# Kernel optimization log

Hardware: AMD Instinct MI355X
Metric: run time of the kernel (lower is better)

Reference implementation:

```python
import math
import jax, jax.numpy as jnp
import numpy as np

BATCH, SEQ, D_MODEL, NUM_HEADS = 4, 2048, 1024, 16
D_K = D_MODEL // NUM_HEADS


def setup_inputs() -> dict:
    key = jax.random.key(0)
    ks = jax.random.split(key, 11)
    s = 0.02
    inp = {
        'encodings_q': jax.random.normal(ks[0], (BATCH, SEQ, D_MODEL), jnp.float32),
        'encodings_k': jax.random.normal(ks[1], (BATCH, SEQ, D_MODEL), jnp.float32),
        'encodings_v': jax.random.normal(ks[2], (BATCH, SEQ, D_MODEL), jnp.float32),
        # causal mask: True = masked out (matches masked_fill semantics)
        'mask': jnp.broadcast_to(jnp.triu(jnp.ones((SEQ, SEQ), bool), k=1),
                                 (BATCH, SEQ, SEQ)),
        'Wq': jax.random.normal(ks[3], (D_MODEL, D_MODEL), jnp.float32) * s,
        'bq': jnp.zeros((D_MODEL,), jnp.float32),
        'Wk': jax.random.normal(ks[4], (D_MODEL, D_MODEL), jnp.float32) * s,
        'bk': jnp.zeros((D_MODEL,), jnp.float32),
        'Wv': jax.random.normal(ks[5], (D_MODEL, D_MODEL), jnp.float32) * s,
        'bv': jnp.zeros((D_MODEL,), jnp.float32),
        'Wo': jax.random.normal(ks[6], (D_MODEL, D_MODEL), jnp.float32) * s,
        'bo': jnp.zeros((D_MODEL,), jnp.float32),
    }
    return inp


def reference(encodings_q, encodings_k, encodings_v, mask,
              Wq, bq, Wk, bk, Wv, bv, Wo, bo):
    B, S, D = encodings_q.shape
    H, Dk = NUM_HEADS, D_K
    # projections (nn.Linear: x @ W.T + b), split heads -> (B, H, S, Dk)
    q = (encodings_q @ Wq.T + bq).reshape(B, S, H, Dk).transpose(0, 2, 1, 3)
    k = (encodings_k @ Wk.T + bk).reshape(B, S, H, Dk).transpose(0, 2, 1, 3)
    v = (encodings_v @ Wv.T + bv).reshape(B, S, H, Dk).transpose(0, 2, 1, 3)
    scores = jnp.einsum('bhqd,bhkd->bhqk', q, k) / math.sqrt(Dk)
    # mask dim == 3 -> unsqueeze head dim; masked_fill(mask, -1e9)
    scores = jnp.where(mask[:, None, :, :], jnp.float32(-1e9), scores)
    weights = jax.nn.softmax(scores, axis=-1)
    attn = jnp.einsum('bhqk,bhkd->bhqd', weights, v)
    attn = attn.transpose(0, 2, 1, 3).reshape(B, S, D)
    return attn @ Wo.T + bo
```

## Files before the change

### kernel.cpp

```cpp
#include <hip/hip_runtime.h>
#include <hip/hip_bf16.h>
#include <cstdint>

typedef __bf16 bf16;
typedef bf16  bf16x4 __attribute__((ext_vector_type(4)));
typedef bf16  bf16x8 __attribute__((ext_vector_type(8)));
typedef float f32x4  __attribute__((ext_vector_type(4)));

#define MFMA16(a, b, c) __builtin_amdgcn_mfma_f32_16x16x32_bf16((a), (b), (c), 0, 0, 0)

constexpr int BATCH = 4;
constexpr int SEQ   = 2048;
constexpr int DM    = 1024;
constexpr int NH    = 16;
constexpr int DK    = 64;

constexpr float QSCALE = 0.125f * 1.44269504088896340736f;

__device__ __forceinline__ void gld_lds16(const void* g, void* l) {
    __builtin_amdgcn_global_load_lds(
        (const __attribute__((address_space(1))) unsigned int*)(uintptr_t)g,
        (__attribute__((address_space(3))) unsigned int*)(uintptr_t)l,
        16, 0, 0);
}

__device__ __forceinline__ bf16x8 cvt8(const float* __restrict__ p) {
    f32x4 a = *(const f32x4*)p;
    f32x4 b = *(const f32x4*)(p + 4);
    bf16x8 r;
    r[0] = (bf16)a[0]; r[1] = (bf16)a[1]; r[2] = (bf16)a[2]; r[3] = (bf16)a[3];
    r[4] = (bf16)b[0]; r[5] = (bf16)b[1]; r[6] = (bf16)b[2]; r[7] = (bf16)b[3];
    return r;
}

__global__ __launch_bounds__(256)
void cvt_all(const float* __restrict__ xq, const float* __restrict__ xk,
             const float* __restrict__ xv,
             const float* __restrict__ wq, const float* __restrict__ wk,
             const float* __restrict__ wv, const float* __restrict__ wo,
             bf16* __restrict__ X3, bf16* __restrict__ WB)
{
    const int bid = blockIdx.x;
    const float* s;
    bf16* d;
    int local;
    if (bid < 12288) {
        const int which = bid >> 12;
        local = bid & 4095;
        s = (which == 0) ? xq : (which == 1) ? xk : xv;
        d = X3 + (size_t)which * ((size_t)BATCH * SEQ * DM);
    } else {
        const int b2 = bid - 12288;
        const int which = b2 >> 9;
        local = b2 & 511;
        s = (which == 0) ? wq : (which == 1) ? wk : (which == 2) ? wv : wo;
        d = WB + (size_t)which * (size_t)(DM * DM);
    }
    const size_t i = ((size_t)local * 256 + threadIdx.x) * 8;
    *(bf16x8*)(d + i) = cvt8(s + i);
}

__global__ __launch_bounds__(256)
void cvt_x(const float* __restrict__ src, bf16* __restrict__ dst) {
    const size_t i = ((size_t)blockIdx.x * 256 + threadIdx.x) * 8;
    *(bf16x8*)(dst + i) = cvt8(src + i);
}

__global__ __launch_bounds__(256)
void cvt_w4(const float* __restrict__ s0, const float* __restrict__ s1,
            const float* __restrict__ s2, const float* __restrict__ s3,
            bf16* __restrict__ dst) {
    const float* s = (blockIdx.y == 0) ? s0 : (blockIdx.y == 1) ? s1
                   : (blockIdx.y == 2) ? s2 : s3;
    const size_t i = ((size_t)blockIdx.x * 256 + threadIdx.x) * 8;
    *(bf16x8*)(dst + (size_t)blockIdx.y * (1024 * 1024) + i) = cvt8(s + i);
}

template <int MODE>
__device__ __forceinline__
void gemm_core(const bf16* __restrict__ A, const bf16* __restrict__ W,
               const float* __restrict__ bias, void* __restrict__ outp,
               int m0, int n0, bf16* As, bf16* Bs, float oscale)
{
    const int tid  = threadIdx.x;
    const int lane = tid & 63;
    const int wave = tid >> 6;
    const int wm   = (wave >> 1) * 64;
    const int wn   = (wave & 1) * 64;
    const int q4   = lane >> 4;
    const int r    = lane & 15;
    const int srow = lane >> 2;
    const int scol = (((lane & 3) ^ ((lane >> 3) & 3)) << 3);

    f32x4 acc[4][4];
#pragma unroll
    for (int i = 0; i < 4; i++)
#pragma unroll
        for (int j = 0; j < 4; j++) acc[i][j] = (f32x4){0.f, 0.f, 0.f, 0.f};

    const bf16* Ag = A + (size_t)(m0 + wave * 32 + srow) * 1024 + scol;
    const bf16* Wg = W + (size_t)(n0 + wave * 32 + srow) * 1024 + scol;
    const int woff = (wave * 32) * 32;
    constexpr int BUF = 128 * 32;

#define GSTAGE(ks, bsel) do {                                        \
        const int _b = (bsel) * BUF + woff;                          \
        gld_lds16(Ag + (ks) * 32,             As + _b);              \
        gld_lds16(Ag + (ks) * 32 + 16 * 1024, As + _b + 16 * 32);   \
        gld_lds16(Wg + (ks) * 32,             Bs + _b);              \
        gld_lds16(Wg + (ks) * 32 + 16 * 1024, Bs + _b + 16 * 32);   \
    } while (0)

    GSTAGE(0, 0);
    GSTAGE(1, 1);

    const int rsw = (r >> 1) & 3;

    int cur = 0, pre = 2;
    for (int t = 0; t < 32; ++t) {
        if (t < 30) {
            asm volatile("s_waitcnt vmcnt(4) lgkmcnt(0)" ::: "memory");
        } else {
            asm volatile("s_waitcnt vmcnt(0) lgkmcnt(0)" ::: "memory");
        }
        __builtin_amdgcn_s_barrier();

        if (t < 30) GSTAGE(t + 2, pre);

        const bf16* Ar = As + cur * BUF;
        const bf16* Br = Bs + cur * BUF;

        bf16x8 af[4], bfr[4];
#pragma unroll
        for (int i = 0; i < 4; i++)
            af[i] = *(const bf16x8*)&Ar[(wm + i * 16 + r) * 32 + ((q4 ^ rsw) << 3)];
#pragma unroll
        for (int j = 0; j < 4; j++)
            bfr[j] = *(const bf16x8*)&Br[(wn + j * 16 + r) * 32 + ((q4 ^ rsw) << 3)];
#pragma unroll
        for (int i = 0; i < 4; i++)
#pragma unroll
            for (int j = 0; j < 4; j++) {
                if (MODE == 2)
                    acc[i][j] = MFMA16(af[i], bfr[j], acc[i][j]);
                else
                    acc[i][j] = MFMA16(bfr[j], af[i], acc[i][j]);
            }

        cur = (cur == 2) ? 0 : cur + 1;
        pre = (pre == 2) ? 0 : pre + 1;
    }
#undef GSTAGE

    if (MODE == 2) {
#pragma unroll
        for (int j = 0; j < 4; j++) {
            const int col = n0 + wn + j * 16 + r;
            const float bv = bias[col];
            const int hh = col >> 6, d = col & 63;
#pragma unroll
            for (int i = 0; i < 4; i++) {
                const int s0 = m0 + wm + i * 16 + q4 * 4;
                const int b = s0 >> 11, s = s0 & 2047;
                bf16x4 ov;
#pragma unroll
                for (int rr = 0; rr < 4; rr++) ov[rr] = (bf16)((acc[i][j][rr] + bv) * oscale);
                *(bf16x4*)&((bf16*)outp)[(((size_t)(b * NH + hh)) * DK + d) * SEQ + s] = ov;
            }
        }
    } else {
#pragma unroll
        for (int j = 0; j < 4; j++) {
            const int col0 = n0 + wn + j * 16 + q4 * 4;
            const f32x4 bv4 = *(const f32x4*)&bias[col0];
#pragma unroll
            for (int i = 0; i < 4; i++) {
                const int row = m0 + wm + i * 16 + r;
                if (MODE == 1) {
                    f32x4 ov = (acc[i][j] + bv4) * oscale;
                    *(f32x4*)&((float*)outp)[(size_t)row * 1024 + col0] = ov;
                } else {
                    const int b = row >> 11, s = row & 2047;
                    const int hh = col0 >> 6, d0 = col0 & 63;
                    bf16x4 ov;
#pragma unroll
                    for (int rr = 0; rr < 4; rr++) ov[rr] = (bf16)((acc[i][j][rr] + bv4[rr]) * oscale);
                    *(bf16x4*)&((bf16*)outp)[(((size_t)(b * NH + hh)) * SEQ + s) * DK + d0] = ov;
                }
            }
        }
    }
}

template <int MODE>
__global__ __launch_bounds__(256)
void gemm_fast(const bf16* __restrict__ A, const bf16* __restrict__ W,
               const float* __restrict__ bias, void* __restrict__ outp, float oscale)
{
    __shared__ __align__(16) bf16 As[3][128 * 32];
    __shared__ __align__(16) bf16 Bs[3][128 * 32];
    gemm_core<MODE>(A, W, bias, outp, blockIdx.x * 128, blockIdx.y * 128,
                    &As[0][0], &Bs[0][0], oscale);
}

__global__ __launch_bounds__(256)
void gemm_qkv(const bf16* __restrict__ X3, const bf16* __restrict__ WB,
              const float* __restrict__ bq, const float* __restrict__ bk,
              const float* __restrict__ bv,
              bf16* __restrict__ Qt, bf16* __restrict__ Kt, bf16* __restrict__ Vt)
{
    __shared__ __align__(16) bf16 As[3][128 * 32];
    __shared__ __align__(16) bf16 Bs[3][128 * 32];
    const int z = blockIdx.z;
    const size_t E = (size_t)BATCH * SEQ * DM, WE = (size_t)DM * DM;
    const bf16* A = X3 + (size_t)z * E;
    const bf16* W = WB + (size_t)z * WE;
    const int m0 = blockIdx.x * 128, n0 = blockIdx.y * 128;
    if (z == 2)
        gemm_core<2>(A, W, bv, Vt, m0, n0, &As[0][0], &Bs[0][0], 1.0f);
    else if (z == 1)
        gemm_core<0>(A, W, bk, Kt, m0, n0, &As[0][0], &Bs[0][0], 1.0f);
    else
        gemm_core<0>(A, W, bq, Qt, m0, n0, &As[0][0], &Bs[0][0], QSCALE);
}

template <int MODE>
__global__ __launch_bounds__(256)
void gemm_slow(const void* __restrict__ Ap, const float* __restrict__ W,
               const float* __restrict__ bias, void* __restrict__ outp, float oscale)
{
    __shared__ __align__(16) bf16 As[128 * 32];
    __shared__ __align__(16) bf16 Bs[128 * 32];

    const int tid  = threadIdx.x;
    const int lane = tid & 63;
    const int wave = tid >> 6;
    const int wm   = (wave >> 1) * 64;
    const int wn   = (wave & 1) * 64;
    const int m0   = blockIdx.y * 128;
    const int n0   = blockIdx.x * 128;
    const int q    = lane >> 4;
    const int r    = lane & 15;
    const int lrow  = tid >> 2;
    const int lcol8 = (tid & 3) * 8;

    f32x4 acc[4][4];
#pragma unroll
    for (int i = 0; i < 4; i++)
#pragma unroll
        for (int j = 0; j < 4; j++) acc[i][j] = (f32x4){0.f, 0.f, 0.f, 0.f};

    for (int k0 = 0; k0 < 1024; k0 += 32) {
        __syncthreads();
        if (MODE != 1) {
            const float* Af = (const float*)Ap;
            *(bf16x8*)&As[lrow * 32 + lcol8] =
                cvt8(&Af[(size_t)(m0 + lrow) * 1024 + k0 + lcol8]);
            *(bf16x8*)&As[(64 + lrow) * 32 + lcol8] =
                cvt8(&Af[(size_t)(m0 + 64 + lrow) * 1024 + k0 + lcol8]);
        } else {
            const bf16* Ab = (const bf16*)Ap;
            *(bf16x8*)&As[lrow * 32 + lcol8] =
                *(const bf16x8*)&Ab[(size_t)(m0 + lrow) * 1024 + k0 + lcol8];
            *(bf16x8*)&As[(64 + lrow) * 32 + lcol8] =
                *(const bf16x8*)&Ab[(size_t)(m0 + 64 + lrow) * 1024 + k0 + lcol8];
        }
        *(bf16x8*)&Bs[lrow * 32 + lcol8] =
            cvt8(&W[(size_t)(n0 + lrow) * 1024 + k0 + lcol8]);
        *(bf16x8*)&Bs[(64 + lrow) * 32 + lcol8] =
            cvt8(&W[(size_t)(n0 + 64 + lrow) * 1024 + k0 + lcol8]);
        __syncthreads();

        bf16x8 af[4], bfr[4];
#pragma unroll
        for (int i = 0; i < 4; i++)
            af[i] = *(const bf16x8*)&As[(wm + i * 16 + r) * 32 + q * 8];
#pragma unroll
        for (int j = 0; j < 4; j++)
            bfr[j] = *(const bf16x8*)&Bs[(wn + j * 16 + r) * 32 + q * 8];
#pragma unroll
        for (int i = 0; i < 4; i++)
#pragma unroll
            for (int j = 0; j < 4; j++)
                acc[i][j] = MFMA16(af[i], bfr[j], acc[i][j]);
    }

#pragma unroll
    for (int j = 0; j < 4; j++) {
        const int col = n0 + wn + j * 16 + r;
        const float bv = bias[col];
#pragma unroll
        for (int i = 0; i < 4; i++) {
#pragma unroll
            for (int rr = 0; rr < 4; rr++) {
                const int row = m0 + wm + i * 16 + q * 4 + rr;
                const float v = (acc[i][j][rr] + bv) * oscale;
                if (MODE == 1) {
                    ((float*)outp)[(size_t)row * 1024 + col] = v;
                } else {
                    const int b = row >> 11, s = row & 2047;
                    const int hh = col >> 6, d = col & 63;
                    if (MODE == 0)
                        ((bf16*)outp)[(((size_t)(b * NH + hh)) * SEQ + s) * DK + d] = (bf16)v;
                    else
                        ((bf16*)outp)[(((size_t)(b * NH + hh)) * DK + d) * SEQ + s] = (bf16)v;
                }
            }
        }
    }
}

__global__ __launch_bounds__(512)
void attn_causal(const bf16* __restrict__ Qt, const bf16* __restrict__ Kt,
                 const bf16* __restrict__ Vtt, bf16* __restrict__ Ob)
{
    __shared__ __align__(16) bf16 Ks[2][64 * 64];
    __shared__ __align__(16) bf16 Vs[2][64 * 64];
    __shared__ __align__(16) bf16 Ps[8][16 * 64];

    const int tid  = threadIdx.x;
    const int lane = tid & 63;
    const int wave = tid >> 6;
    const int q4   = lane >> 4;
    const int r    = lane & 15;

    const int bh = blockIdx.x;
    const int yy = (SEQ / 128 - 1) - blockIdx.y;
    const int qb = yy * 128;
    const int b  = bh >> 4;
    const int h  = bh & 15;

    const bf16* Qp = Qt  + ((size_t)bh * SEQ + qb + wave * 16) * DK;
    const bf16* Kp = Kt  + (size_t)bh * SEQ * DK;
    const bf16* Vp = Vtt + (size_t)bh * DK * SEQ;

    const bf16x8 qf0 = *(const bf16x8*)&Qp[r * DK + q4 * 8];
    const bf16x8 qf1 = *(const bf16x8*)&Qp[r * DK + 32 + q4 * 8];

    bf16x8 ones;
#pragma unroll
    for (int j = 0; j < 8; j++) ones[j] = (bf16)1.0f;

    f32x4 o[4], o5;
#pragma unroll
    for (int i = 0; i < 4; i++) o[i] = (f32x4){0.f, 0.f, 0.f, 0.f};
    o5 = (f32x4){0.f, 0.f, 0.f, 0.f};
    float m_i = -1e30f;

    const int nT   = yy * 2 + 2;
    const int qrow = qb + wave * 16 + r;

    const int srow = wave * 8 + (lane >> 3);
    const int scol = ((lane & 7) ^ (srow & 7)) * 8;
    const bf16* KgA = Kp + (size_t)srow * DK + scol;
    const bf16* VgA = Vp + (size_t)srow * SEQ + scol;

    const int sw    = r & 7;
    const int koffA = r * 64 + ((q4)     ^ sw) * 8;
    const int koffB = r * 64 + ((q4 + 4) ^ sw) * 8;

    const int pwr = r * 64;

    {
        gld_lds16(KgA, &Ks[0][wave * 512]);
        gld_lds16(VgA, &Vs[0][wave * 512]);
        KgA += 64 * DK;
        VgA += 64;
    }

    int nbuf = 0;
    for (int t = 0; t < nT; ++t) {
        __syncthreads();

        const bf16* Kb = Ks[nbuf];
        const bf16* Vb = Vs[nbuf];

        if (t + 1 < nT) {
            gld_lds16(KgA, &Ks[nbuf ^ 1][wave * 512]);
            gld_lds16(VgA, &Vs[nbuf ^ 1][wave * 512]);
            KgA += 64 * DK;
            VgA += 64;
        }

        f32x4 s[4];
        __builtin_amdgcn_s_setprio(1);
#pragma unroll
        for (int n = 0; n < 4; n++) {
            bf16x8 k0 = *(const bf16x8*)&Kb[koffA + n * 1024];
            bf16x8 k1 = *(const bf16x8*)&Kb[koffB + n * 1024];
            f32x4 a = (f32x4){0.f, 0.f, 0.f, 0.f};
            a = MFMA16(k0, qf0, a);
            a = MFMA16(k1, qf1, a);
            s[n] = a;
        }
        __builtin_amdgcn_s_setprio(0);

        const int kb = t * 64;
        float mx = -1e30f;
        if (t >= nT - 2) {
#pragma unroll
            for (int n = 0; n < 4; n++) {
                const int c0 = kb + n * 16 + q4 * 4;
#pragma unroll
                for (int rr = 0; rr < 4; rr++) {
                    if (c0 + rr > qrow) s[n][rr] = -1e30f;
                    mx = fmaxf(mx, s[n][rr]);
                }
            }
        } else {
#pragma unroll
            for (int n = 0; n < 4; n++)
#pragma unroll
                for (int rr = 0; rr < 4; rr++)
                    mx = fmaxf(mx, s[n][rr]);
        }
        mx = fmaxf(mx, __shfl_xor(mx, 16, 64));
        mx = fmaxf(mx, __shfl_xor(mx, 32, 64));

        if (__any(mx > m_i + 8.0f)) {
            const float mn    = fmaxf(m_i, mx);
            const float alpha = __builtin_amdgcn_exp2f(m_i - mn);
            m_i = mn;
#pragma unroll
            for (int n = 0; n < 4; n++)
#pragma unroll
                for (int rr = 0; rr < 4; rr++)
                    o[n][rr] *= alpha;
#pragma unroll
            for (int rr = 0; rr < 4; rr++) o5[rr] *= alpha;
        }

        bf16* Pw = &Ps[wave][0];
#pragma unroll
        for (int n = 0; n < 4; n++) {
            bf16x4 pv;
#pragma unroll
            for (int rr = 0; rr < 4; rr++)
                pv[rr] = (bf16)__builtin_amdgcn_exp2f(s[n][rr] - m_i);
            *(bf16x4*)&Pw[pwr + (((n * 4 + q4) ^ ((r & 7) << 1)) << 2)] = pv;
        }
        asm volatile("s_waitcnt lgkmcnt(0)" ::: "memory");

        __builtin_amdgcn_s_setprio(1);
#pragma unroll
        for (int kk = 0; kk < 2; kk++) {
            bf16x8 pf = *(const bf16x8*)&Pw[pwr + (((kk * 4 + q4) ^ (r & 7)) << 3)];
            const int vo = (kk == 0) ? koffA : koffB;
#pragma unroll
            for (int n = 0; n < 4; n++) {
                bf16x8 vf = *(const bf16x8*)&Vb[vo + n * 1024];
                o[n] = MFMA16(vf, pf, o[n]);
            }
            o5 = MFMA16(ones, pf, o5);
        }
        __builtin_amdgcn_s_setprio(0);

        nbuf ^= 1;
    }

    const float inv = 1.0f / o5[0];
#pragma unroll
    for (int n = 0; n < 4; n++) {
        bf16x4 ov;
#pragma unroll
        for (int rr = 0; rr < 4; rr++) ov[rr] = (bf16)(o[n][rr] * inv);
        *(bf16x4*)&Ob[((size_t)b * SEQ + qrow) * DM + h * DK + n * 16 + q4 * 4] = ov;
    }
}

extern "C" void kernel_launch(void* const* d_in, const int* in_sizes, int n_in,
                              void* d_out, int out_size, void* d_ws, size_t ws_size,
                              hipStream_t stream)
{
    const float* xq = (const float*)d_in[0];
    const float* xk = (const float*)d_in[1];
    const float* xv = (const float*)d_in[2];
    const float* Wq = (const float*)d_in[4];
    const float* bq = (const float*)d_in[5];
    const float* Wk = (const float*)d_in[6];
    const float* bk = (const float*)d_in[7];
    const float* Wv = (const float*)d_in[8];
    const float* bv = (const float*)d_in[9];
    const float* Wo = (const float*)d_in[10];
    const float* bo = (const float*)d_in[11];

    const size_t E  = (size_t)BATCH * SEQ * DM;
    const size_t WE = (size_t)DM * DM;
    bf16* Qt = (bf16*)d_ws;
    bf16* Kt = Qt + E;
    bf16* Vt = Kt + E;
    bf16* Ab = Vt + E;

    dim3 gblk(256);
    dim3 ablk(512);
    dim3 agrid(BATCH * NH, SEQ / 128);

    const size_t need_fused = (7 * E + 4 * WE) * sizeof(bf16);
    const size_t need_fast  = (5 * E + 4 * WE) * sizeof(bf16);

    if (ws_size >= need_fused) {
        bf16* X3 = Ab + E;
        bf16* WB = X3 + 3 * E;

        cvt_all<<<dim3(14336), gblk, 0, stream>>>(xq, xk, xv, Wq, Wk, Wv, Wo, X3, WB);

        gemm_qkv<<<dim3(64, 8, 3), gblk, 0, stream>>>(X3, WB, bq, bk, bv, Qt, Kt, Vt);

        attn_causal<<<agrid, ablk, 0, stream>>>(Qt, Kt, Vt, Ab);

        gemm_fast<1><<<dim3(64, 8), gblk, 0, stream>>>(Ab, WB + 3 * WE, bo, d_out, 1.0f);
    } else if (ws_size >= need_fast) {
        bf16* X  = Ab + E;
        bf16* WB = X + E;

        cvt_w4<<<dim3(512, 4), gblk, 0, stream>>>(Wq, Wk, Wv, Wo, WB);

        cvt_x<<<dim3(4096), gblk, 0, stream>>>(xq, X);
        gemm_fast<0><<<dim3(64, 8), gblk, 0, stream>>>(X, WB + 0 * WE, bq, Qt, QSCALE);
        cvt_x<<<dim3(4096), gblk, 0, stream>>>(xk, X);
        gemm_fast<0><<<dim3(64, 8), gblk, 0, stream>>>(X, WB + 1 * WE, bk, Kt, 1.0f);
        cvt_x<<<dim3(4096), gblk, 0, stream>>>(xv, X);
        gemm_fast<2><<<dim3(64, 8), gblk, 0, stream>>>(X, WB + 2 * WE, bv, Vt, 1.0f);

        attn_causal<<<agrid, ablk, 0, stream>>>(Qt, Kt, Vt, Ab);

        gemm_fast<1><<<dim3(64, 8), gblk, 0, stream>>>(Ab, WB + 3 * WE, bo, d_out, 1.0f);
    } else {
        dim3 ggrid_s(DM / 128, (BATCH * SEQ) / 128);
        gemm_slow<0><<<ggrid_s, gblk, 0, stream>>>(xq, Wq, bq, Qt, QSCALE);
        gemm_slow<0><<<ggrid_s, gblk, 0, stream>>>(xk, Wk, bk, Kt, 1.0f);
        gemm_slow<2><<<ggrid_s, gblk, 0, stream>>>(xv, Wv, bv, Vt, 1.0f);
        attn_causal<<<agrid, ablk, 0, stream>>>(Qt, Kt, Vt, Ab);
        gemm_slow<1><<<ggrid_s, gblk, 0, stream>>>(Ab, Wo, bo, d_out, 1.0f);
    }
}
```

Before: 339.3 us.

## Pre-tile weights in k-blocked layout and load B fragments straight to registers

The weight conversion kernels now write bf16 weights in a k-blocked layout of 32-wide K slabs, each holding all 1024 rows contiguously. The GEMM core can then load B fragments directly from global memory into registers with a three-deep register pipeline, and the LDS staging for B is removed. This halves LDS traffic and footprint per block, which may help occupancy, but each wave issues its own global loads for B with no sharing across waves, and register pressure goes up. The vmcnt wait counts were adjusted to match the new number of outstanding loads.

```diff
diff --git a/kernel.cpp b/kernel.cpp
--- a/kernel.cpp
+++ b/kernel.cpp
@@ -33,6 +33,7 @@
     return r;
 }
 
+
 __global__ __launch_bounds__(256)
 void cvt_all(const float* __restrict__ xq, const float* __restrict__ xk,
              const float* __restrict__ xv,
@@ -41,23 +42,26 @@
              bf16* __restrict__ X3, bf16* __restrict__ WB)
 {
     const int bid = blockIdx.x;
-    const float* s;
-    bf16* d;
-    int local;
     if (bid < 12288) {
         const int which = bid >> 12;
-        local = bid & 4095;
-        s = (which == 0) ? xq : (which == 1) ? xk : xv;
-        d = X3 + (size_t)which * ((size_t)BATCH * SEQ * DM);
+        const int local = bid & 4095;
+        const float* s = (which == 0) ? xq : (which == 1) ? xk : xv;
+        bf16* d = X3 + (size_t)which * ((size_t)BATCH * SEQ * DM);
+        const size_t i = ((size_t)local * 256 + threadIdx.x) * 8;
+        *(bf16x8*)(d + i) = cvt8(s + i);
     } else {
         const int b2 = bid - 12288;
         const int which = b2 >> 9;
-        local = b2 & 511;
-        s = (which == 0) ? wq : (which == 1) ? wk : (which == 2) ? wv : wo;
-        d = WB + (size_t)which * (size_t)(DM * DM);
-    }
-    const size_t i = ((size_t)local * 256 + threadIdx.x) * 8;
-    *(bf16x8*)(d + i) = cvt8(s + i);
+        const int local = b2 & 511;
+        const float* s = (which == 0) ? wq : (which == 1) ? wk
+                       : (which == 2) ? wv : wo;
+        bf16* d = WB + (size_t)which * (size_t)(DM * DM);
+        const size_t i = ((size_t)local * 256 + threadIdx.x) * 8;
+        const int n = (int)(i >> 10);
+        const int k = (int)(i & 1023);
+        const size_t off = ((size_t)(k >> 5) << 15) + ((size_t)n << 5) + (k & 31);
+        *(bf16x8*)(d + off) = cvt8(s + i);
+    }
 }
 
 __global__ __launch_bounds__(256)
@@ -73,14 +77,17 @@
     const float* s = (blockIdx.y == 0) ? s0 : (blockIdx.y == 1) ? s1
                    : (blockIdx.y == 2) ? s2 : s3;
     const size_t i = ((size_t)blockIdx.x * 256 + threadIdx.x) * 8;
-    *(bf16x8*)(dst + (size_t)blockIdx.y * (1024 * 1024) + i) = cvt8(s + i);
+    const int n = (int)(i >> 10);
+    const int k = (int)(i & 1023);
+    const size_t off = ((size_t)(k >> 5) << 15) + ((size_t)n << 5) + (k & 31);
+    *(bf16x8*)(dst + (size_t)blockIdx.y * (1024 * 1024) + off) = cvt8(s + i);
 }
 
 template <int MODE>
 __device__ __forceinline__
-void gemm_core(const bf16* __restrict__ A, const bf16* __restrict__ W,
+void gemm_core(const bf16* __restrict__ A, const bf16* __restrict__ Wf,
                const float* __restrict__ bias, void* __restrict__ outp,
-               int m0, int n0, bf16* As, bf16* Bs, float oscale)
+               int m0, int n0, bf16* As, float oscale)
 {
     const int tid  = threadIdx.x;
     const int lane = tid & 63;
@@ -99,58 +106,65 @@
         for (int j = 0; j < 4; j++) acc[i][j] = (f32x4){0.f, 0.f, 0.f, 0.f};
 
     const bf16* Ag = A + (size_t)(m0 + wave * 32 + srow) * 1024 + scol;
-    const bf16* Wg = W + (size_t)(n0 + wave * 32 + srow) * 1024 + scol;
+    const bf16* Bg = Wf + (size_t)(n0 + wn + r) * 32 + q4 * 8;
     const int woff = (wave * 32) * 32;
     constexpr int BUF = 128 * 32;
 
-#define GSTAGE(ks, bsel) do {                                        \
+#define ASTAGE(ks, bsel) do {                                        \
         const int _b = (bsel) * BUF + woff;                          \
         gld_lds16(Ag + (ks) * 32,             As + _b);              \
         gld_lds16(Ag + (ks) * 32 + 16 * 1024, As + _b + 16 * 32);   \
-        gld_lds16(Wg + (ks) * 32,             Bs + _b);              \
-        gld_lds16(Wg + (ks) * 32 + 16 * 1024, Bs + _b + 16 * 32);   \
     } while (0)
 
-    GSTAGE(0, 0);
-    GSTAGE(1, 1);
+    bf16x8 b0[4], b1[4], b2[4];
+
+    ASTAGE(0, 0);
+#pragma unroll
+    for (int j = 0; j < 4; j++) b0[j] = *(const bf16x8*)&Bg[j * 512];
+    ASTAGE(1, 1);
+#pragma unroll
+    for (int j = 0; j < 4; j++) b1[j] = *(const bf16x8*)&Bg[32768 + j * 512];
 
     const int rsw = (r >> 1) & 3;
 
     int cur = 0, pre = 2;
     for (int t = 0; t < 32; ++t) {
-        if (t < 30) {
-            asm volatile("s_waitcnt vmcnt(4) lgkmcnt(0)" ::: "memory");
+        if (t < 31) {
+            asm volatile("s_waitcnt vmcnt(6) lgkmcnt(0)" ::: "memory");
         } else {
             asm volatile("s_waitcnt vmcnt(0) lgkmcnt(0)" ::: "memory");
         }
         __builtin_amdgcn_s_barrier();
 
-        if (t < 30) GSTAGE(t + 2, pre);
+        if (t < 30) {
+            ASTAGE(t + 2, pre);
+#pragma unroll
+            for (int j = 0; j < 4; j++)
+                b2[j] = *(const bf16x8*)&Bg[(size_t)(t + 2) * 32768 + j * 512];
+        }
 
         const bf16* Ar = As + cur * BUF;
-        const bf16* Br = Bs + cur * BUF;
-
-        bf16x8 af[4], bfr[4];
+        bf16x8 af[4];
 #pragma unroll
         for (int i = 0; i < 4; i++)
             af[i] = *(const bf16x8*)&Ar[(wm + i * 16 + r) * 32 + ((q4 ^ rsw) << 3)];
 #pragma unroll
-        for (int j = 0; j < 4; j++)
-            bfr[j] = *(const bf16x8*)&Br[(wn + j * 16 + r) * 32 + ((q4 ^ rsw) << 3)];
-#pragma unroll
         for (int i = 0; i < 4; i++)
 #pragma unroll
             for (int j = 0; j < 4; j++) {
                 if (MODE == 2)
-                    acc[i][j] = MFMA16(af[i], bfr[j], acc[i][j]);
+                    acc[i][j] = MFMA16(af[i], b0[j], acc[i][j]);
                 else
-                    acc[i][j] = MFMA16(bfr[j], af[i], acc[i][j]);
+                    acc[i][j] = MFMA16(b0[j], af[i], acc[i][j]);
             }
+
+#pragma unroll
+        for (int j = 0; j < 4; j++) { b0[j] = b1[j]; b1[j] = b2[j]; }
 
         cur = (cur == 2) ? 0 : cur + 1;
         pre = (pre == 2) ? 0 : pre + 1;
     }
-#undef GSTAGE
+#undef ASTAGE
 
     if (MODE == 2) {
 #pragma unroll
@@ -198,9 +212,8 @@
                const float* __restrict__ bias, void* __restrict__ outp, float oscale)
 {
     __shared__ __align__(16) bf16 As[3][128 * 32];
-    __shared__ __align__(16) bf16 Bs[3][128 * 32];
     gemm_core<MODE>(A, W, bias, outp, blockIdx.x * 128, blockIdx.y * 128,
-                    &As[0][0], &Bs[0][0], oscale);
+                    &As[0][0], oscale);
 }
 
 __global__ __launch_bounds__(256)
@@ -210,18 +223,17 @@
               bf16* __restrict__ Qt, bf16* __restrict__ Kt, bf16* __restrict__ Vt)
 {
     __shared__ __align__(16) bf16 As[3][128 * 32];
-    __shared__ __align__(16) bf16 Bs[3][128 * 32];
     const int z = blockIdx.z;
     const size_t E = (size_t)BATCH * SEQ * DM, WE = (size_t)DM * DM;
     const bf16* A = X3 + (size_t)z * E;
     const bf16* W = WB + (size_t)z * WE;
     const int m0 = blockIdx.x * 128, n0 = blockIdx.y * 128;
     if (z == 2)
-        gemm_core<2>(A, W, bv, Vt, m0, n0, &As[0][0], &Bs[0][0], 1.0f);
+        gemm_core<2>(A, W, bv, Vt, m0, n0, &As[0][0], 1.0f);
     else if (z == 1)
-        gemm_core<0>(A, W, bk, Kt, m0, n0, &As[0][0], &Bs[0][0], 1.0f);
+        gemm_core<0>(A, W, bk, Kt, m0, n0, &As[0][0], 1.0f);
     else
-        gemm_core<0>(A, W, bq, Qt, m0, n0, &As[0][0], &Bs[0][0], QSCALE);
+        gemm_core<0>(A, W, bq, Qt, m0, n0, &As[0][0], QSCALE);
 }
 
 template <int MODE>
```

New measurement: 344.6 us. About the same (+1.5%).

## Enlarge GEMM tiles to 128x256 with 512 threads and double-buffered K=64 stages

Applied to the files above, without the earlier changes.

Reworks the bf16 GEMM core from 128x128 tiles with 4 waves and a triple-buffered K=32 pipeline to 128x256 tiles with 8 waves. Each stage now covers K=64, split into two halves, and uses double buffering in one combined LDS array for A and W rows. s_setprio is raised around the MFMA block. The goal is better operand reuse per loaded byte and fewer barriers per K step. In exchange the grid has half as many blocks, and the larger LDS footprint may lower occupancy.

```diff
diff --git a/kernel.cpp b/kernel.cpp
--- a/kernel.cpp
+++ b/kernel.cpp
@@ -80,17 +80,18 @@
 __device__ __forceinline__
 void gemm_core(const bf16* __restrict__ A, const bf16* __restrict__ W,
                const float* __restrict__ bias, void* __restrict__ outp,
-               int m0, int n0, bf16* As, bf16* Bs, float oscale)
+               int m0, int n0, bf16* Lb, float oscale)
 {
     const int tid  = threadIdx.x;
     const int lane = tid & 63;
     const int wave = tid >> 6;
-    const int wm   = (wave >> 1) * 64;
-    const int wn   = (wave & 1) * 64;
+    const int wm   = (wave >> 2) * 64;
+    const int wn   = (wave & 3) * 64;
     const int q4   = lane >> 4;
     const int r    = lane & 15;
-    const int srow = lane >> 2;
-    const int scol = (((lane & 3) ^ ((lane >> 3) & 3)) << 3);
+
+    constexpr int KH    = 384 * 32;
+    constexpr int BUFSZ = 2 * KH;
 
     f32x4 acc[4][4];
 #pragma unroll
@@ -98,59 +99,68 @@
 #pragma unroll
         for (int j = 0; j < 4; j++) acc[i][j] = (f32x4){0.f, 0.f, 0.f, 0.f};
 
-    const bf16* Ag = A + (size_t)(m0 + wave * 32 + srow) * 1024 + scol;
-    const bf16* Wg = W + (size_t)(n0 + wave * 32 + srow) * 1024 + scol;
-    const int woff = (wave * 32) * 32;
-    constexpr int BUF = 128 * 32;
-
-#define GSTAGE(ks, bsel) do {                                        \
-        const int _b = (bsel) * BUF + woff;                          \
-        gld_lds16(Ag + (ks) * 32,             As + _b);              \
-        gld_lds16(Ag + (ks) * 32 + 16 * 1024, As + _b + 16 * 32);   \
-        gld_lds16(Wg + (ks) * 32,             Bs + _b);              \
-        gld_lds16(Wg + (ks) * 32 + 16 * 1024, Bs + _b + 16 * 32);   \
+    const int srow_l = lane >> 2;
+    const int scol   = (((lane & 3) ^ ((lane >> 3) & 3)) << 3);
+    const bf16* srcc[3];
+    int ldsc[3];
+#pragma unroll
+    for (int c = 0; c < 3; c++) {
+        const int rowb = wave * 48 + c * 16;
+        const int row  = rowb + srow_l;
+        srcc[c] = ((row < 128) ? (A + (size_t)(m0 + row) * 1024)
+                               : (W + (size_t)(n0 + row - 128) * 1024)) + scol;
+        ldsc[c] = rowb * 32;
+    }
+
+#define STAGE_HALF(ks, kh, buf) do {                                         \
+        bf16* _d = Lb + (buf) * BUFSZ + (kh) * KH;                           \
+        gld_lds16(srcc[0] + (ks) * 64 + (kh) * 32, _d + ldsc[0]);            \
+        gld_lds16(srcc[1] + (ks) * 64 + (kh) * 32, _d + ldsc[1]);            \
+        gld_lds16(srcc[2] + (ks) * 64 + (kh) * 32, _d + ldsc[2]);            \
     } while (0)
 
-    GSTAGE(0, 0);
-    GSTAGE(1, 1);
+    STAGE_HALF(0, 0, 0);
+    STAGE_HALF(0, 1, 0);
 
     const int rsw = (r >> 1) & 3;
-
-    int cur = 0, pre = 2;
-    for (int t = 0; t < 32; ++t) {
-        if (t < 30) {
-            asm volatile("s_waitcnt vmcnt(4) lgkmcnt(0)" ::: "memory");
-        } else {
-            asm volatile("s_waitcnt vmcnt(0) lgkmcnt(0)" ::: "memory");
-        }
-        __builtin_amdgcn_s_barrier();
-
-        if (t < 30) GSTAGE(t + 2, pre);
-
-        const bf16* Ar = As + cur * BUF;
-        const bf16* Br = Bs + cur * BUF;
-
-        bf16x8 af[4], bfr[4];
-#pragma unroll
-        for (int i = 0; i < 4; i++)
-            af[i] = *(const bf16x8*)&Ar[(wm + i * 16 + r) * 32 + ((q4 ^ rsw) << 3)];
-#pragma unroll
-        for (int j = 0; j < 4; j++)
-            bfr[j] = *(const bf16x8*)&Br[(wn + j * 16 + r) * 32 + ((q4 ^ rsw) << 3)];
-#pragma unroll
-        for (int i = 0; i < 4; i++)
-#pragma unroll
-            for (int j = 0; j < 4; j++) {
-                if (MODE == 2)
-                    acc[i][j] = MFMA16(af[i], bfr[j], acc[i][j]);
-                else
-                    acc[i][j] = MFMA16(bfr[j], af[i], acc[i][j]);
-            }
-
-        cur = (cur == 2) ? 0 : cur + 1;
-        pre = (pre == 2) ? 0 : pre + 1;
-    }
-#undef GSTAGE
+    const int xsl = ((q4 ^ rsw) << 3);
+
+    int cur = 0;
+    for (int t = 0; t < 16; ++t) {
+#pragma unroll
+        for (int kh = 0; kh < 2; ++kh) {
+            if (t == 15 && kh == 1)
+                asm volatile("s_waitcnt vmcnt(0)" ::: "memory");
+            else
+                asm volatile("s_waitcnt vmcnt(3)" ::: "memory");
+            __builtin_amdgcn_s_barrier();
+
+            if (t < 15) STAGE_HALF(t + 1, kh, cur ^ 1);
+
+            const bf16* Lr = Lb + cur * BUFSZ + kh * KH;
+            bf16x8 af[4], bfr[4];
+#pragma unroll
+            for (int i = 0; i < 4; i++)
+                af[i] = *(const bf16x8*)&Lr[(wm + i * 16 + r) * 32 + xsl];
+#pragma unroll
+            for (int j = 0; j < 4; j++)
+                bfr[j] = *(const bf16x8*)&Lr[(128 + wn + j * 16 + r) * 32 + xsl];
+
+            __builtin_amdgcn_s_setprio(1);
+#pragma unroll
+            for (int i = 0; i < 4; i++)
+#pragma unroll
+                for (int j = 0; j < 4; j++) {
+                    if (MODE == 2)
+                        acc[i][j] = MFMA16(af[i], bfr[j], acc[i][j]);
+                    else
+                        acc[i][j] = MFMA16(bfr[j], af[i], acc[i][j]);
+                }
+            __builtin_amdgcn_s_setprio(0);
+        }
+        cur ^= 1;
+    }
+#undef STAGE_HALF
 
     if (MODE == 2) {
 #pragma unroll
@@ -193,35 +203,33 @@
 }
 
 template <int MODE>
-__global__ __launch_bounds__(256)
+__global__ __launch_bounds__(512)
 void gemm_fast(const bf16* __restrict__ A, const bf16* __restrict__ W,
                const float* __restrict__ bias, void* __restrict__ outp, float oscale)
 {
-    __shared__ __align__(16) bf16 As[3][128 * 32];
-    __shared__ __align__(16) bf16 Bs[3][128 * 32];
-    gemm_core<MODE>(A, W, bias, outp, blockIdx.x * 128, blockIdx.y * 128,
-                    &As[0][0], &Bs[0][0], oscale);
-}
-
-__global__ __launch_bounds__(256)
+    __shared__ __align__(16) bf16 L[2 * 2 * 384 * 32];
+    gemm_core<MODE>(A, W, bias, outp, blockIdx.x * 128, blockIdx.y * 256,
+                    &L[0], oscale);
+}
+
+__global__ __launch_bounds__(512)
 void gemm_qkv(const bf16* __restrict__ X3, const bf16* __restrict__ WB,
               const float* __restrict__ bq, const float* __restrict__ bk,
               const float* __restrict__ bv,
               bf16* __restrict__ Qt, bf16* __restrict__ Kt, bf16* __restrict__ Vt)
 {
-    __shared__ __align__(16) bf16 As[3][128 * 32];
-    __shared__ __align__(16) bf16 Bs[3][128 * 32];
+    __shared__ __align__(16) bf16 L[2 * 2 * 384 * 32];
     const int z = blockIdx.z;
     const size_t E = (size_t)BATCH * SEQ * DM, WE = (size_t)DM * DM;
     const bf16* A = X3 + (size_t)z * E;
     const bf16* W = WB + (size_t)z * WE;
-    const int m0 = blockIdx.x * 128, n0 = blockIdx.y * 128;
+    const int m0 = blockIdx.x * 128, n0 = blockIdx.y * 256;
     if (z == 2)
-        gemm_core<2>(A, W, bv, Vt, m0, n0, &As[0][0], &Bs[0][0], 1.0f);
+        gemm_core<2>(A, W, bv, Vt, m0, n0, &L[0], 1.0f);
     else if (z == 1)
-        gemm_core<0>(A, W, bk, Kt, m0, n0, &As[0][0], &Bs[0][0], 1.0f);
+        gemm_core<0>(A, W, bk, Kt, m0, n0, &L[0], 1.0f);
     else
-        gemm_core<0>(A, W, bq, Qt, m0, n0, &As[0][0], &Bs[0][0], QSCALE);
+        gemm_core<0>(A, W, bq, Qt, m0, n0, &L[0], QSCALE);
 }
 
 template <int MODE>
@@ -492,6 +500,8 @@
     bf16* Ab = Vt + E;
 
     dim3 gblk(256);
+    dim3 mblk(512);
+    dim3 ggrid(64, 4);
     dim3 ablk(512);
     dim3 agrid(BATCH * NH, SEQ / 128);
 
@@ -504,11 +514,11 @@
 
         cvt_all<<<dim3(14336), gblk, 0, stream>>>(xq, xk, xv, Wq, Wk, Wv, Wo, X3, WB);
 
-        gemm_qkv<<<dim3(64, 8, 3), gblk, 0, stream>>>(X3, WB, bq, bk, bv, Qt, Kt, Vt);
+        gemm_qkv<<<dim3(64, 4, 3), mblk, 0, stream>>>(X3, WB, bq, bk, bv, Qt, Kt, Vt);
 
         attn_causal<<<agrid, ablk, 0, stream>>>(Qt, Kt, Vt, Ab);
 
-        gemm_fast<1><<<dim3(64, 8), gblk, 0, stream>>>(Ab, WB + 3 * WE, bo, d_out, 1.0f);
+        gemm_fast<1><<<ggrid, mblk, 0, stream>>>(Ab, WB + 3 * WE, bo, d_out, 1.0f);
     } else if (ws_size >= need_fast) {
         bf16* X  = Ab + E;
         bf16* WB = X + E;
@@ -516,15 +526,15 @@
         cvt_w4<<<dim3(512, 4), gblk, 0, stream>>>(Wq, Wk, Wv, Wo, WB);
 
         cvt_x<<<dim3(4096), gblk, 0, stream>>>(xq, X);
-        gemm_fast<0><<<dim3(64, 8), gblk, 0, stream>>>(X, WB + 0 * WE, bq, Qt, QSCALE);
+        gemm_fast<0><<<ggrid, mblk, 0, stream>>>(X, WB + 0 * WE, bq, Qt, QSCALE);
         cvt_x<<<dim3(4096), gblk, 0, stream>>>(xk, X);
-        gemm_fast<0><<<dim3(64, 8), gblk, 0, stream>>>(X, WB + 1 * WE, bk, Kt, 1.0f);
+        gemm_fast<0><<<ggrid, mblk, 0, stream>>>(X, WB + 1 * WE, bk, Kt, 1.0f);
         cvt_x<<<dim3(4096), gblk, 0, stream>>>(xv, X);
-        gemm_fast<2><<<dim3(64, 8), gblk, 0, stream>>>(X, WB + 2 * WE, bv, Vt, 1.0f);
+        gemm_fast<2><<<ggrid, mblk, 0, stream>>>(X, WB + 2 * WE, bv, Vt, 1.0f);
 
         attn_causal<<<agrid, ablk, 0, stream>>>(Qt, Kt, Vt, Ab);
 
-        gemm_fast<1><<<dim3(64, 8), gblk, 0, stream>>>(Ab, WB + 3 * WE, bo, d_out, 1.0f);
+        gemm_fast<1><<<ggrid, mblk, 0, stream>>>(Ab, WB + 3 * WE, bo, d_out, 1.0f);
     } else {
         dim3 ggrid_s(DM / 128, (BATCH * SEQ) / 128);
         gemm_slow<0><<<ggrid_s, gblk, 0, stream>>>(xq, Wq, bq, Qt, QSCALE);
```

New measurement: 336.8 us. About the same (-0.8%).
